# Kernel optimization log

Measured on AMD Instinct MI355X. Metric: run time of the kernel, lower is better.

## Reference

```python
import jax, jax.numpy as jnp
import numpy as np

D = 32          # latent_dim
ALPHA = 3.0


def setup_inputs() -> dict:
    key = jax.random.key(0)
    ks = jax.random.split(key, 8)
    B, N, T = 4, 2048, 288
    spatial_nodes = jax.random.normal(ks[0], (B, N, D), dtype=jnp.float32)
    temporal_nodes = jax.random.normal(ks[1], (B, T, D), dtype=jnp.float32)
    # ss graph params: Linear(D, D, bias=False) x2
    W_ss1 = jax.random.normal(ks[2], (D, D), dtype=jnp.float32) / np.sqrt(D)
    W_ss2 = jax.random.normal(ks[3], (D, D), dtype=jnp.float32) / np.sqrt(D)
    # st / ts relation MLPs: Linear(2D, 1) -> weight vector (2D,) + scalar bias
    w_st = jax.random.normal(ks[4], (2 * D,), dtype=jnp.float32) / np.sqrt(2 * D)
    b_st = jnp.zeros((), dtype=jnp.float32)
    w_ts = jax.random.normal(ks[5], (2 * D,), dtype=jnp.float32) / np.sqrt(2 * D)
    b_ts = jnp.zeros((), dtype=jnp.float32)
    return {
        "spatial_nodes": spatial_nodes,
        "temporal_nodes": temporal_nodes,
        "W_ss1": W_ss1,
        "W_ss2": W_ss2,
        "w_st": w_st,
        "b_st": b_st,
        "w_ts": w_ts,
        "b_ts": b_ts,
    }


def _pair_linear(x1, x2, w, b):
    """Linear(2D->1) over the concat of every (x1[n], x2[m]) pair, without
    materializing the [B, N1, N2, 2D] tiled tensor: splits the weight into
    two matvecs and a broadcast add. Same math as the torch tile+concat+Linear."""
    d = x1.shape[-1]
    s1 = x1 @ w[:d]   # [B, N1]
    s2 = x2 @ w[d:]   # [B, N2]
    return s1[:, :, None] + s2[:, None, :] + b  # [B, N1, N2]


def reference(spatial_nodes, temporal_nodes, W_ss1, W_ss2, w_st, b_st, w_ts, b_ts):
    B, N, d = spatial_nodes.shape
    T = temporal_nodes.shape[1]

    # base graph: inner products of all node embeddings (only tt block survives)
    node_embs = jnp.concatenate([spatial_nodes, temporal_nodes], axis=1)  # [B, N+T, D]
    adj = jnp.einsum('bnf,bmf->bnm', node_embs, node_embs)               # [B, N+T, N+T]

    # ss block: antisymmetric tanh graph (nn.Linear applies x @ W.T)
    nv1 = jnp.tanh(ALPHA * (spatial_nodes @ W_ss1.T))
    nv2 = jnp.tanh(ALPHA * (spatial_nodes @ W_ss2.T))
    m = jnp.einsum('bnf,bmf->bnm', nv1, nv2)
    ss_adj = jnp.tanh(m - jnp.swapaxes(m, 1, 2))

    # st / ts blocks: pairwise concat + Linear(2D->1), fused
    st_adj = _pair_linear(spatial_nodes, temporal_nodes, w_st, b_st)  # [B, N, T]
    ts_adj = _pair_linear(temporal_nodes, spatial_nodes, w_ts, b_ts)  # [B, T, N]

    adj = adj.at[:, :N, N:].set(st_adj)
    adj = adj.at[:, N:, :N].set(ts_adj)
    adj = adj.at[:, :N, :N].set(ss_adj)

    # tt_mask=True: upper-triangular (incl. diagonal) on the temporal-temporal block
    adj = adj.at[:, N:, N:].set(jnp.triu(adj[:, N:, N:]))

    # forward: tanh(relu(adj)). The per-batch nonzero edge extraction in the
    # torch code is a dense->COO repack of exactly this tensor (indices where
    # adj != 0, values = adj at those indices); the dense adj is the canonical
    adj = jnp.tanh(jax.nn.relu(adj))
    return adj
```

## Files before the change

kernel.cpp:

```cpp
#include <hip/hip_runtime.h>

#define NTOT 2336
#define NS   2048
#define NT   288
#define DD   32
#define BATCH 4
#define S2   ((size_t)NTOT * NTOT)
#define LDSS 68

#define WS_NV2   (BATCH * NS * DD)
#define WS_SST1  (2 * BATCH * NS * DD)
#define WS_SST2  (WS_SST1 + BATCH * NS)
#define WS_STS1  (WS_SST2 + BATCH * NT)
#define WS_STS2  (WS_STS1 + BATCH * NT)

__device__ __forceinline__ float fast_tanh(float x) {
    float e = __expf(2.0f * x);
    return 1.0f - 2.0f * __builtin_amdgcn_rcpf(e + 1.0f);
}
__device__ __forceinline__ float f_out(float x) {
    return fast_tanh(fmaxf(x, 0.0f));
}

__global__ void precompute_kernel(const float* __restrict__ S,
                                  const float* __restrict__ T,
                                  const float* __restrict__ W1,
                                  const float* __restrict__ W2,
                                  const float* __restrict__ w_st,
                                  const float* __restrict__ b_st,
                                  const float* __restrict__ w_ts,
                                  const float* __restrict__ b_ts,
                                  float* __restrict__ ws) {
    __shared__ float sW1[DD * DD];
    __shared__ float sW2[DD * DD];
    __shared__ float swst[2 * DD];
    __shared__ float swts[2 * DD];
    int tid = threadIdx.x;
    for (int i = tid; i < DD * DD; i += 256) { sW1[i] = W1[i]; sW2[i] = W2[i]; }
    if (tid < 2 * DD) { swst[tid] = w_st[tid]; swts[tid] = w_ts[tid]; }
    __syncthreads();

    float* nv1   = ws;
    float* nv2   = ws + WS_NV2;
    float* s_st1 = ws + WS_SST1;
    float* s_st2 = ws + WS_SST2;
    float* s_ts1 = ws + WS_STS1;
    float* s_ts2 = ws + WS_STS2;

    int idx = blockIdx.x * 256 + tid;
    if (idx < BATCH * NS) {
        const float* row = S + idx * DD;
        float r[DD];
        #pragma unroll
        for (int q = 0; q < 8; q++) {
            float4 v = ((const float4*)row)[q];
            r[q * 4 + 0] = v.x; r[q * 4 + 1] = v.y;
            r[q * 4 + 2] = v.z; r[q * 4 + 3] = v.w;
        }
        float o1[DD], o2[DD];
        for (int d = 0; d < DD; d++) {
            float a1 = 0.f, a2 = 0.f;
            #pragma unroll
            for (int k = 0; k < DD; k++) {
                a1 = fmaf(r[k], sW1[d * DD + k], a1);
                a2 = fmaf(r[k], sW2[d * DD + k], a2);
            }
            o1[d] = fast_tanh(3.0f * a1);
            o2[d] = fast_tanh(3.0f * a2);
        }
        #pragma unroll
        for (int q = 0; q < 8; q++) {
            float4 v1 = { o1[q*4], o1[q*4+1], o1[q*4+2], o1[q*4+3] };
            float4 v2 = { o2[q*4], o2[q*4+1], o2[q*4+2], o2[q*4+3] };
            ((float4*)(nv1 + idx * DD))[q] = v1;
            ((float4*)(nv2 + idx * DD))[q] = v2;
        }
        float d1 = 0.f, d2 = 0.f;
        #pragma unroll
        for (int k = 0; k < DD; k++) {
            d1 = fmaf(r[k], swst[k], d1);
            d2 = fmaf(r[k], swts[DD + k], d2);
        }
        s_st1[idx] = d1 + b_st[0];
        s_ts2[idx] = d2;
    } else if (idx < BATCH * NS + BATCH * NT) {
        int t = idx - BATCH * NS;
        const float* row = T + t * DD;
        float r[DD];
        #pragma unroll
        for (int q = 0; q < 8; q++) {
            float4 v = ((const float4*)row)[q];
            r[q * 4 + 0] = v.x; r[q * 4 + 1] = v.y;
            r[q * 4 + 2] = v.z; r[q * 4 + 3] = v.w;
        }
        float d1 = 0.f, d2 = 0.f;
        #pragma unroll
        for (int k = 0; k < DD; k++) {
            d1 = fmaf(r[k], swst[DD + k], d1);
            d2 = fmaf(r[k], swts[k], d2);
        }
        s_st2[t] = d1;
        s_ts1[t] = d2 + b_ts[0];
    }
}

__global__ __launch_bounds__(256, 4) void ss_kernel(const float* __restrict__ nv1,
                                                    const float* __restrict__ nv2,
                                                    float* __restrict__ out) {
    int ti = blockIdx.x, tj = blockIdx.y, b = blockIdx.z;
    if (tj < ti) return;

    __shared__ __align__(16) float A1[DD][LDSS];
    __shared__ __align__(16) float A2[DD][LDSS];
    __shared__ __align__(16) float B1[DD][LDSS];
    __shared__ __align__(16) float B2[DD][LDSS];

    int tid = threadIdx.x;
    const float* src1 = nv1 + ((size_t)b * NS + ti * 64) * DD;
    const float* src2 = nv2 + ((size_t)b * NS + ti * 64) * DD;
    const float* src3 = nv2 + ((size_t)b * NS + tj * 64) * DD;
    const float* src4 = nv1 + ((size_t)b * NS + tj * 64) * DD;

    #pragma unroll
    for (int rep = 0; rep < 2; rep++) {
        int q   = rep * 256 + tid;
        int row = q >> 3;
        int k4  = (q & 7) * 4;
        float4 v;
        v = *(const float4*)(src1 + row * DD + k4);
        A1[k4+0][row] = v.x; A1[k4+1][row] = v.y; A1[k4+2][row] = v.z; A1[k4+3][row] = v.w;
        v = *(const float4*)(src2 + row * DD + k4);
        A2[k4+0][row] = v.x; A2[k4+1][row] = v.y; A2[k4+2][row] = v.z; A2[k4+3][row] = v.w;
        v = *(const float4*)(src3 + row * DD + k4);
        B1[k4+0][row] = v.x; B1[k4+1][row] = v.y; B1[k4+2][row] = v.z; B1[k4+3][row] = v.w;
        v = *(const float4*)(src4 + row * DD + k4);
        B2[k4+0][row] = v.x; B2[k4+1][row] = v.y; B2[k4+2][row] = v.z; B2[k4+3][row] = v.w;
    }
    __syncthreads();

    int tx = tid & 15, ty = tid >> 4;
    int r0 = ty * 4, c0 = tx * 4;

    float acc[4][4] = {};
    #pragma unroll
    for (int k = 0; k < DD; k++) {
        float4 a1 = *(const float4*)&A1[k][r0];
        float4 b1 = *(const float4*)&B1[k][c0];
        float4 a2 = *(const float4*)&A2[k][r0];
        float4 b2 = *(const float4*)&B2[k][c0];
        float a1v[4] = { a1.x, a1.y, a1.z, a1.w };
        float b1v[4] = { b1.x, b1.y, b1.z, b1.w };
        float a2v[4] = { a2.x, a2.y, a2.z, a2.w };
        float b2v[4] = { b2.x, b2.y, b2.z, b2.w };
        #pragma unroll
        for (int i = 0; i < 4; i++)
            #pragma unroll
            for (int j = 0; j < 4; j++) {
                acc[i][j] = fmaf(a1v[i],  b1v[j], acc[i][j]);
                acc[i][j] = fmaf(-a2v[i], b2v[j], acc[i][j]);
            }
    }

    float t[4][4];
    #pragma unroll
    for (int i = 0; i < 4; i++)
        #pragma unroll
        for (int j = 0; j < 4; j++)
            t[i][j] = fast_tanh(acc[i][j]);

    float* obase = out + (size_t)b * S2;
    #pragma unroll
    for (int i = 0; i < 4; i++) {
        float4 v = { f_out(t[i][0]), f_out(t[i][1]), f_out(t[i][2]), f_out(t[i][3]) };
        *(float4*)(obase + (size_t)(ti * 64 + r0 + i) * NTOT + tj * 64 + c0) = v;
    }
    if (ti != tj) {
        #pragma unroll
        for (int j = 0; j < 4; j++) {
            float4 v = { f_out(-t[0][j]), f_out(-t[1][j]), f_out(-t[2][j]), f_out(-t[3][j]) };
            *(float4*)(obase + (size_t)(tj * 64 + c0 + j) * NTOT + ti * 64 + r0) = v;
        }
    }
}

__global__ void st_kernel(const float* __restrict__ ws, float* __restrict__ out) {
    const float* s_st1 = ws + WS_SST1;
    const float* s_st2 = ws + WS_SST2;
    int idx = blockIdx.x * 256 + threadIdx.x;
    if (idx >= BATCH * NS * (NT / 4)) return;
    int t4  = idx % (NT / 4);
    int row = idx / (NT / 4);
    int b   = row >> 11;
    int n   = row & (NS - 1);
    float  s1 = s_st1[row];
    float4 s2 = *(const float4*)(s_st2 + b * NT + t4 * 4);
    float4 v  = { f_out(s1 + s2.x), f_out(s1 + s2.y), f_out(s1 + s2.z), f_out(s1 + s2.w) };
    *(float4*)(out + (size_t)b * S2 + (size_t)n * NTOT + NS + t4 * 4) = v;
}

__global__ void ts_kernel(const float* __restrict__ ws, float* __restrict__ out) {
    const float* s_ts1 = ws + WS_STS1;
    const float* s_ts2 = ws + WS_STS2;
    int idx = blockIdx.x * 256 + threadIdx.x;
    if (idx >= BATCH * NT * (NS / 4)) return;
    int n4  = idx & 511;
    int row = idx >> 9;
    int b   = row / NT;
    int t   = row - b * NT;
    float  s1 = s_ts1[row];
    float4 s2 = *(const float4*)(s_ts2 + b * NS + n4 * 4);
    float4 v  = { f_out(s1 + s2.x), f_out(s1 + s2.y), f_out(s1 + s2.z), f_out(s1 + s2.w) };
    *(float4*)(out + (size_t)b * S2 + (size_t)(NS + t) * NTOT + n4 * 4) = v;
}

__global__ void tt_kernel(const float* __restrict__ T, float* __restrict__ out) {
    int idx = blockIdx.x * 256 + threadIdx.x;
    if (idx >= BATCH * NT * NT) return;
    int j   = idx % NT;
    int rem = idx / NT;
    int i   = rem % NT;
    int b   = rem / NT;
    float o = 0.f;
    if (j >= i) {
        const float4* ri = (const float4*)(T + (b * NT + i) * DD);
        const float4* rj = (const float4*)(T + (b * NT + j) * DD);
        float acc = 0.f;
        #pragma unroll
        for (int q = 0; q < 8; q++) {
            float4 a = ri[q], c = rj[q];
            acc = fmaf(a.x, c.x, acc); acc = fmaf(a.y, c.y, acc);
            acc = fmaf(a.z, c.z, acc); acc = fmaf(a.w, c.w, acc);
        }
        o = f_out(acc);
    }
    out[(size_t)b * S2 + (size_t)(NS + i) * NTOT + NS + j] = o;
}

extern "C" void kernel_launch(void* const* d_in, const int* in_sizes, int n_in,
                              void* d_out, int out_size, void* d_ws, size_t ws_size,
                              hipStream_t stream) {
    const float* S    = (const float*)d_in[0];
    const float* T    = (const float*)d_in[1];
    const float* W1   = (const float*)d_in[2];
    const float* W2   = (const float*)d_in[3];
    const float* w_st = (const float*)d_in[4];
    const float* b_st = (const float*)d_in[5];
    const float* w_ts = (const float*)d_in[6];
    const float* b_ts = (const float*)d_in[7];
    float* out = (float*)d_out;
    float* ws  = (float*)d_ws;

    precompute_kernel<<<37, 256, 0, stream>>>(S, T, W1, W2, w_st, b_st, w_ts, b_ts, ws);
    ss_kernel<<<dim3(32, 32, BATCH), 256, 0, stream>>>(ws, ws + WS_NV2, out);
    st_kernel<<<2304, 256, 0, stream>>>(ws, out);
    ts_kernel<<<2304, 256, 0, stream>>>(ws, out);
    tt_kernel<<<1296, 256, 0, stream>>>((const float*)d_in[1], out);
}
```

Baseline: 162.1 us.

## Merge output kernels into one launch with 128-tile ss blocks and transposed nv layout

The ss, st, ts and tt output kernels are folded into a single mega kernel that dispatches work by block index, removing three launches and their tails. The ss part now uses 128x128 tiles over upper-triangular tile pairs only, so no blocks launch just to exit. Each thread computes an 8x8 register tile with two 16-deep K phases. The precompute kernel writes nv1/nv2 transposed (feature-major) so tiles load into shared memory with plain float4 copies instead of scattered transposing stores. The bigger accumulator tile raises register pressure and lowers occupancy, and the strided transposed writes in precompute cost extra.

```diff
diff --git a/kernel.cpp b/kernel.cpp
--- a/kernel.cpp
+++ b/kernel.cpp
@@ -6,13 +6,22 @@
 #define DD   32
 #define BATCH 4
 #define S2   ((size_t)NTOT * NTOT)
-#define LDSS 68
 
 #define WS_NV2   (BATCH * NS * DD)
 #define WS_SST1  (2 * BATCH * NS * DD)
 #define WS_SST2  (WS_SST1 + BATCH * NS)
 #define WS_STS1  (WS_SST2 + BATCH * NT)
 #define WS_STS2  (WS_STS1 + BATCH * NT)
+
+#define TILE   128
+#define NTILE  (NS / TILE)
+#define NPAIR  (NTILE * (NTILE + 1) / 2)
+#define SS_BLOCKS (NPAIR * BATCH)
+#define ST_BLOCKS 2304
+#define TS_BLOCKS 2304
+#define TT_BLOCKS 1296
+#define GRID_BLOCKS (SS_BLOCKS + ST_BLOCKS + TS_BLOCKS + TT_BLOCKS)
+#define LDST 136
 
 __device__ __forceinline__ float fast_tanh(float x) {
     float e = __expf(2.0f * x);
@@ -40,8 +49,8 @@
     if (tid < 2 * DD) { swst[tid] = w_st[tid]; swts[tid] = w_ts[tid]; }
     __syncthreads();
 
-    float* nv1   = ws;
-    float* nv2   = ws + WS_NV2;
+    float* nv1T  = ws;
+    float* nv2T  = ws + WS_NV2;
     float* s_st1 = ws + WS_SST1;
     float* s_st2 = ws + WS_SST2;
     float* s_ts1 = ws + WS_STS1;
@@ -49,6 +58,7 @@
 
     int idx = blockIdx.x * 256 + tid;
     if (idx < BATCH * NS) {
+        int b = idx >> 11, n = idx & (NS - 1);
         const float* row = S + idx * DD;
         float r[DD];
         #pragma unroll
@@ -57,7 +67,8 @@
             r[q * 4 + 0] = v.x; r[q * 4 + 1] = v.y;
             r[q * 4 + 2] = v.z; r[q * 4 + 3] = v.w;
         }
-        float o1[DD], o2[DD];
+        size_t base = (size_t)b * DD * NS + n;
+        #pragma unroll
         for (int d = 0; d < DD; d++) {
             float a1 = 0.f, a2 = 0.f;
             #pragma unroll
@@ -65,15 +76,8 @@
                 a1 = fmaf(r[k], sW1[d * DD + k], a1);
                 a2 = fmaf(r[k], sW2[d * DD + k], a2);
             }
-            o1[d] = fast_tanh(3.0f * a1);
-            o2[d] = fast_tanh(3.0f * a2);
-        }
-        #pragma unroll
-        for (int q = 0; q < 8; q++) {
-            float4 v1 = { o1[q*4], o1[q*4+1], o1[q*4+2], o1[q*4+3] };
-            float4 v2 = { o2[q*4], o2[q*4+1], o2[q*4+2], o2[q*4+3] };
-            ((float4*)(nv1 + idx * DD))[q] = v1;
-            ((float4*)(nv2 + idx * DD))[q] = v2;
+            nv1T[base + (size_t)d * NS] = fast_tanh(3.0f * a1);
+            nv2T[base + (size_t)d * NS] = fast_tanh(3.0f * a2);
         }
         float d1 = 0.f, d2 = 0.f;
         #pragma unroll
@@ -104,136 +108,140 @@
     }
 }
 
-__global__ __launch_bounds__(256, 4) void ss_kernel(const float* __restrict__ nv1,
-                                                    const float* __restrict__ nv2,
-                                                    float* __restrict__ out) {
-    int ti = blockIdx.x, tj = blockIdx.y, b = blockIdx.z;
-    if (tj < ti) return;
-
-    __shared__ __align__(16) float A1[DD][LDSS];
-    __shared__ __align__(16) float A2[DD][LDSS];
-    __shared__ __align__(16) float B1[DD][LDSS];
-    __shared__ __align__(16) float B2[DD][LDSS];
-
+__global__ __launch_bounds__(256) void mega_kernel(const float* __restrict__ ws,
+                                                   const float* __restrict__ T,
+                                                   float* __restrict__ out) {
+    __shared__ __align__(16) float sA1[16][LDST];
+    __shared__ __align__(16) float sA2[16][LDST];
+    __shared__ __align__(16) float sB1[16][LDST];
+    __shared__ __align__(16) float sB2[16][LDST];
+
+    int blk = blockIdx.x;
     int tid = threadIdx.x;
-    const float* src1 = nv1 + ((size_t)b * NS + ti * 64) * DD;
-    const float* src2 = nv2 + ((size_t)b * NS + ti * 64) * DD;
-    const float* src3 = nv2 + ((size_t)b * NS + tj * 64) * DD;
-    const float* src4 = nv1 + ((size_t)b * NS + tj * 64) * DD;
-
-    #pragma unroll
-    for (int rep = 0; rep < 2; rep++) {
-        int q   = rep * 256 + tid;
-        int row = q >> 3;
-        int k4  = (q & 7) * 4;
-        float4 v;
-        v = *(const float4*)(src1 + row * DD + k4);
-        A1[k4+0][row] = v.x; A1[k4+1][row] = v.y; A1[k4+2][row] = v.z; A1[k4+3][row] = v.w;
-        v = *(const float4*)(src2 + row * DD + k4);
-        A2[k4+0][row] = v.x; A2[k4+1][row] = v.y; A2[k4+2][row] = v.z; A2[k4+3][row] = v.w;
-        v = *(const float4*)(src3 + row * DD + k4);
-        B1[k4+0][row] = v.x; B1[k4+1][row] = v.y; B1[k4+2][row] = v.z; B1[k4+3][row] = v.w;
-        v = *(const float4*)(src4 + row * DD + k4);
-        B2[k4+0][row] = v.x; B2[k4+1][row] = v.y; B2[k4+2][row] = v.z; B2[k4+3][row] = v.w;
+
+    if (blk < SS_BLOCKS) {
+        int b = blk & 3;
+        int p = blk >> 2;
+        int ti = 0;
+        while (p >= NTILE - ti) { p -= NTILE - ti; ti++; }
+        int tj = ti + p;
+
+        const float* nv1T = ws + (size_t)b * DD * NS;
+        const float* nv2T = ws + WS_NV2 + (size_t)b * DD * NS;
+
+        int tx = tid & 15, ty = tid >> 4;
+        float acc[8][8] = {};
+
+        #pragma unroll
+        for (int ph = 0; ph < 2; ph++) {
+            if (ph) __syncthreads();
+            #pragma unroll
+            for (int it = 0; it < 2; it++) {
+                int idx = it * 256 + tid;
+                int k   = idx >> 5;
+                int c4  = (idx & 31) * 4;
+                const float* g = nv1T + (size_t)(ph * 16 + k) * NS;
+                const float* h = nv2T + (size_t)(ph * 16 + k) * NS;
+                *(float4*)&sA1[k][c4] = *(const float4*)(g + ti * TILE + c4);
+                *(float4*)&sA2[k][c4] = *(const float4*)(h + ti * TILE + c4);
+                *(float4*)&sB1[k][c4] = *(const float4*)(h + tj * TILE + c4);
+                *(float4*)&sB2[k][c4] = *(const float4*)(g + tj * TILE + c4);
+            }
+            __syncthreads();
+            #pragma unroll
+            for (int k = 0; k < 16; k++) {
+                float4 a1l = *(const float4*)&sA1[k][ty * 4];
+                float4 a1h = *(const float4*)&sA1[k][64 + ty * 4];
+                float4 a2l = *(const float4*)&sA2[k][ty * 4];
+                float4 a2h = *(const float4*)&sA2[k][64 + ty * 4];
+                float4 b1l = *(const float4*)&sB1[k][tx * 4];
+                float4 b1h = *(const float4*)&sB1[k][64 + tx * 4];
+                float4 b2l = *(const float4*)&sB2[k][tx * 4];
+                float4 b2h = *(const float4*)&sB2[k][64 + tx * 4];
+                float av1[8] = { a1l.x,a1l.y,a1l.z,a1l.w, a1h.x,a1h.y,a1h.z,a1h.w };
+                float av2[8] = { a2l.x,a2l.y,a2l.z,a2l.w, a2h.x,a2h.y,a2h.z,a2h.w };
+                float bv1[8] = { b1l.x,b1l.y,b1l.z,b1l.w, b1h.x,b1h.y,b1h.z,b1h.w };
+                float bv2[8] = { b2l.x,b2l.y,b2l.z,b2l.w, b2h.x,b2h.y,b2h.z,b2h.w };
+                #pragma unroll
+                for (int i = 0; i < 8; i++)
+                    #pragma unroll
+                    for (int j = 0; j < 8; j++) {
+                        acc[i][j] = fmaf(av1[i],  bv1[j], acc[i][j]);
+                        acc[i][j] = fmaf(-av2[i], bv2[j], acc[i][j]);
+                    }
+            }
+        }
+
+        #pragma unroll
+        for (int i = 0; i < 8; i++)
+            #pragma unroll
+            for (int j = 0; j < 8; j++)
+                acc[i][j] = fast_tanh(acc[i][j]);
+
+        float* obase = out + (size_t)b * S2;
+        #pragma unroll
+        for (int i = 0; i < 8; i++) {
+            int r = ti * TILE + ((i < 4) ? (ty * 4 + i) : (60 + ty * 4 + i));
+            float4 v0 = { f_out(acc[i][0]), f_out(acc[i][1]), f_out(acc[i][2]), f_out(acc[i][3]) };
+            float4 v1 = { f_out(acc[i][4]), f_out(acc[i][5]), f_out(acc[i][6]), f_out(acc[i][7]) };
+            *(float4*)(obase + (size_t)r * NTOT + tj * TILE + tx * 4)      = v0;
+            *(float4*)(obase + (size_t)r * NTOT + tj * TILE + 64 + tx * 4) = v1;
+        }
+        if (ti != tj) {
+            #pragma unroll
+            for (int j = 0; j < 8; j++) {
+                int r = tj * TILE + ((j < 4) ? (tx * 4 + j) : (60 + tx * 4 + j));
+                float4 v0 = { f_out(-acc[0][j]), f_out(-acc[1][j]), f_out(-acc[2][j]), f_out(-acc[3][j]) };
+                float4 v1 = { f_out(-acc[4][j]), f_out(-acc[5][j]), f_out(-acc[6][j]), f_out(-acc[7][j]) };
+                *(float4*)(obase + (size_t)r * NTOT + ti * TILE + ty * 4)      = v0;
+                *(float4*)(obase + (size_t)r * NTOT + ti * TILE + 64 + ty * 4) = v1;
+            }
+        }
+    } else if (blk < SS_BLOCKS + ST_BLOCKS) {
+        const float* s_st1 = ws + WS_SST1;
+        const float* s_st2 = ws + WS_SST2;
+        int idx = (blk - SS_BLOCKS) * 256 + tid;
+        int t4  = idx % (NT / 4);
+        int row = idx / (NT / 4);
+        int b   = row >> 11;
+        int n   = row & (NS - 1);
+        float  s1 = s_st1[row];
+        float4 s2 = *(const float4*)(s_st2 + b * NT + t4 * 4);
+        float4 v  = { f_out(s1 + s2.x), f_out(s1 + s2.y), f_out(s1 + s2.z), f_out(s1 + s2.w) };
+        *(float4*)(out + (size_t)b * S2 + (size_t)n * NTOT + NS + t4 * 4) = v;
+    } else if (blk < SS_BLOCKS + ST_BLOCKS + TS_BLOCKS) {
+        const float* s_ts1 = ws + WS_STS1;
+        const float* s_ts2 = ws + WS_STS2;
+        int idx = (blk - SS_BLOCKS - ST_BLOCKS) * 256 + tid;
+        int n4  = idx & 511;
+        int row = idx >> 9;
+        int b   = row / NT;
+        int t   = row - b * NT;
+        float  s1 = s_ts1[row];
+        float4 s2 = *(const float4*)(s_ts2 + b * NS + n4 * 4);
+        float4 v  = { f_out(s1 + s2.x), f_out(s1 + s2.y), f_out(s1 + s2.z), f_out(s1 + s2.w) };
+        *(float4*)(out + (size_t)b * S2 + (size_t)(NS + t) * NTOT + n4 * 4) = v;
+    } else {
+        int idx = (blk - SS_BLOCKS - ST_BLOCKS - TS_BLOCKS) * 256 + tid;
+        int j   = idx % NT;
+        int rem = idx / NT;
+        int i   = rem % NT;
+        int b   = rem / NT;
+        float o = 0.f;
+        if (j >= i) {
+            const float4* ri = (const float4*)(T + (b * NT + i) * DD);
+            const float4* rj = (const float4*)(T + (b * NT + j) * DD);
+            float acc = 0.f;
+            #pragma unroll
+            for (int q = 0; q < 8; q++) {
+                float4 a = ri[q], c = rj[q];
+                acc = fmaf(a.x, c.x, acc); acc = fmaf(a.y, c.y, acc);
+                acc = fmaf(a.z, c.z, acc); acc = fmaf(a.w, c.w, acc);
+            }
+            o = f_out(acc);
+        }
+        out[(size_t)b * S2 + (size_t)(NS + i) * NTOT + NS + j] = o;
     }
-    __syncthreads();
-
-    int tx = tid & 15, ty = tid >> 4;
-    int r0 = ty * 4, c0 = tx * 4;
-
-    float acc[4][4] = {};
-    #pragma unroll
-    for (int k = 0; k < DD; k++) {
-        float4 a1 = *(const float4*)&A1[k][r0];
-        float4 b1 = *(const float4*)&B1[k][c0];
-        float4 a2 = *(const float4*)&A2[k][r0];
-        float4 b2 = *(const float4*)&B2[k][c0];
-        float a1v[4] = { a1.x, a1.y, a1.z, a1.w };
-        float b1v[4] = { b1.x, b1.y, b1.z, b1.w };
-        float a2v[4] = { a2.x, a2.y, a2.z, a2.w };
-        float b2v[4] = { b2.x, b2.y, b2.z, b2.w };
-        #pragma unroll
-        for (int i = 0; i < 4; i++)
-            #pragma unroll
-            for (int j = 0; j < 4; j++) {
-                acc[i][j] = fmaf(a1v[i],  b1v[j], acc[i][j]);
-                acc[i][j] = fmaf(-a2v[i], b2v[j], acc[i][j]);
-            }
-    }
-
-    float t[4][4];
-    #pragma unroll
-    for (int i = 0; i < 4; i++)
-        #pragma unroll
-        for (int j = 0; j < 4; j++)
-            t[i][j] = fast_tanh(acc[i][j]);
-
-    float* obase = out + (size_t)b * S2;
-    #pragma unroll
-    for (int i = 0; i < 4; i++) {
-        float4 v = { f_out(t[i][0]), f_out(t[i][1]), f_out(t[i][2]), f_out(t[i][3]) };
-        *(float4*)(obase + (size_t)(ti * 64 + r0 + i) * NTOT + tj * 64 + c0) = v;
-    }
-    if (ti != tj) {
-        #pragma unroll
-        for (int j = 0; j < 4; j++) {
-            float4 v = { f_out(-t[0][j]), f_out(-t[1][j]), f_out(-t[2][j]), f_out(-t[3][j]) };
-            *(float4*)(obase + (size_t)(tj * 64 + c0 + j) * NTOT + ti * 64 + r0) = v;
-        }
-    }
-}
-
-__global__ void st_kernel(const float* __restrict__ ws, float* __restrict__ out) {
-    const float* s_st1 = ws + WS_SST1;
-    const float* s_st2 = ws + WS_SST2;
-    int idx = blockIdx.x * 256 + threadIdx.x;
-    if (idx >= BATCH * NS * (NT / 4)) return;
-    int t4  = idx % (NT / 4);
-    int row = idx / (NT / 4);
-    int b   = row >> 11;
-    int n   = row & (NS - 1);
-    float  s1 = s_st1[row];
-    float4 s2 = *(const float4*)(s_st2 + b * NT + t4 * 4);
-    float4 v  = { f_out(s1 + s2.x), f_out(s1 + s2.y), f_out(s1 + s2.z), f_out(s1 + s2.w) };
-    *(float4*)(out + (size_t)b * S2 + (size_t)n * NTOT + NS + t4 * 4) = v;
-}
-
-__global__ void ts_kernel(const float* __restrict__ ws, float* __restrict__ out) {
-    const float* s_ts1 = ws + WS_STS1;
-    const float* s_ts2 = ws + WS_STS2;
-    int idx = blockIdx.x * 256 + threadIdx.x;
-    if (idx >= BATCH * NT * (NS / 4)) return;
-    int n4  = idx & 511;
-    int row = idx >> 9;
-    int b   = row / NT;
-    int t   = row - b * NT;
-    float  s1 = s_ts1[row];
-    float4 s2 = *(const float4*)(s_ts2 + b * NS + n4 * 4);
-    float4 v  = { f_out(s1 + s2.x), f_out(s1 + s2.y), f_out(s1 + s2.z), f_out(s1 + s2.w) };
-    *(float4*)(out + (size_t)b * S2 + (size_t)(NS + t) * NTOT + n4 * 4) = v;
-}
-
-__global__ void tt_kernel(const float* __restrict__ T, float* __restrict__ out) {
-    int idx = blockIdx.x * 256 + threadIdx.x;
-    if (idx >= BATCH * NT * NT) return;
-    int j   = idx % NT;
-    int rem = idx / NT;
-    int i   = rem % NT;
-    int b   = rem / NT;
-    float o = 0.f;
-    if (j >= i) {
-        const float4* ri = (const float4*)(T + (b * NT + i) * DD);
-        const float4* rj = (const float4*)(T + (b * NT + j) * DD);
-        float acc = 0.f;
-        #pragma unroll
-        for (int q = 0; q < 8; q++) {
-            float4 a = ri[q], c = rj[q];
-            acc = fmaf(a.x, c.x, acc); acc = fmaf(a.y, c.y, acc);
-            acc = fmaf(a.z, c.z, acc); acc = fmaf(a.w, c.w, acc);
-        }
-        o = f_out(acc);
-    }
-    out[(size_t)b * S2 + (size_t)(NS + i) * NTOT + NS + j] = o;
 }
 
 extern "C" void kernel_launch(void* const* d_in, const int* in_sizes, int n_in,
@@ -251,8 +259,5 @@
     float* ws  = (float*)d_ws;
 
     precompute_kernel<<<37, 256, 0, stream>>>(S, T, W1, W2, w_st, b_st, w_ts, b_ts, ws);
-    ss_kernel<<<dim3(32, 32, BATCH), 256, 0, stream>>>(ws, ws + WS_NV2, out);
-    st_kernel<<<2304, 256, 0, stream>>>(ws, out);
-    ts_kernel<<<2304, 256, 0, stream>>>(ws, out);
-    tt_kernel<<<1296, 256, 0, stream>>>((const float*)d_in[1], out);
-}
+    mega_kernel<<<GRID_BLOCKS, 256, 0, stream>>>(ws, T, out);
+}
```

After: 138.7 us. -14.5%, faster.
